# Performance work log

Measured on AMD Instinct MI355X. Metric: run time of the kernel, lower is better.

Reference implementation:

```python
import jax, jax.numpy as jnp
import numpy as np
from jax import lax

B, C, H, W = 2, 64, 192, 192
KS = 3
N = KS * KS
L = 3  # num_gdns (ResBlocks)


def conv2d(x, w, b=None, padding=0):
    out = lax.conv_general_dilated(x, w, (1, 1), [(padding, padding)] * 2,
                                   dimension_numbers=('NCHW', 'OIHW', 'NCHW'))
    if b is not None:
        out = out + b[None, :, None, None]
    return out


def gdn(x, beta, gamma):
    # y = x / sqrt(beta + sum_j gamma_ij x_j^2)  (inverse=False)
    norm = conv2d(x * x, gamma[:, :, None, None], beta)
    return x / jnp.sqrt(norm)


def resblock(x, w1, w2, beta, gamma):
    res = x
    h = jax.nn.celu(gdn(conv2d(x, w1, padding=0), beta, gamma))  # conv1: no pad (H-2)
    return conv2d(h, w2, padding=2) + res  # conv2: pad 2 restores H


def deform_conv(x, offset, w_dc):
    # DCNv1 (pure-pytorch impl): offset (b,2N,h,w), rows first then cols.
    b, c, Hh, Ww = x.shape
    h, w = offset.shape[2], offset.shape[3]
    pad = 1
    xp = jnp.pad(x, ((0, 0), (0, 0), (pad, pad), (pad, pad)))
    Hp, Wp = Hh + 2 * pad, Ww + 2 * pad
    r = (KS - 1) // 2
    knr, knc = jnp.meshgrid(jnp.arange(-r, r + 1), jnp.arange(-r, r + 1), indexing='ij')
    p_n = jnp.concatenate([knr.reshape(-1), knc.reshape(-1)]).astype(x.dtype)  # (2N,)
    gr, gc = jnp.meshgrid(jnp.arange(1, h + 1), jnp.arange(1, w + 1), indexing='ij')
    p0 = jnp.concatenate([jnp.broadcast_to(gr[None], (N, h, w)),
                          jnp.broadcast_to(gc[None], (N, h, w))], 0).astype(x.dtype)  # (2N,h,w)
    p = p0[None] + p_n[None, :, None, None] + offset  # (b,2N,h,w)
    p = jnp.transpose(p, (0, 2, 3, 1))  # (b,h,w,2N)
    pr = jnp.clip(p[..., :N], 0, Hp - 1)
    pc = jnp.clip(p[..., N:], 0, Wp - 1)
    q0 = lax.stop_gradient(jnp.floor(p))
    qr0 = jnp.clip(q0[..., :N], 0, Hp - 1).astype(jnp.int32)
    qc0 = jnp.clip(q0[..., N:], 0, Wp - 1).astype(jnp.int32)
    qr1 = jnp.clip(q0[..., :N] + 1, 0, Hp - 1).astype(jnp.int32)
    qc1 = jnp.clip(q0[..., N:] + 1, 0, Wp - 1).astype(jnp.int32)
    # bilinear weights (match torch impl exactly)
    g_lt = (1 + (qr0 - pr)) * (1 + (qc0 - pc))
    g_rb = (1 - (qr1 - pr)) * (1 - (qc1 - pc))
    g_lb = (1 + (qr0 - pr)) * (1 - (qc1 - pc))
    g_rt = (1 - (qr1 - pr)) * (1 + (qc0 - pc))
    xf = xp.reshape(b, c, Hp * Wp)

    def gather(qr, qc):
        idx = (qr * Wp + qc).reshape(b, -1)  # (b, h*w*N)
        g = jax.vmap(lambda xb, ib: xb[:, ib])(xf, idx)  # (b,c,h*w*N)
        return g.reshape(b, c, h, w, N)

    xo = (g_lt[:, None] * gather(qr0, qc0) + g_rb[:, None] * gather(qr1, qc1)
          + g_lb[:, None] * gather(qr0, qc1) + g_rt[:, None] * gather(qr1, qc0))
    # stride-ks conv over reshaped x_offset == contraction over (c, n)
    wf = w_dc.reshape(w_dc.shape[0], c, N)
    return jnp.einsum('bchwn,ocn->bohw', xo, wf)


def setup_inputs() -> dict:
    key = jax.random.key(0)
    ks = jax.random.split(key, 11)
    f_r = jax.random.normal(ks[0], (B, C, H, W), jnp.float32)
    m_t = jax.random.normal(ks[1], (B, C, H, W), jnp.float32)
    w_pconv = jax.random.normal(ks[2], (2 * N, C, KS, KS), jnp.float32) * 0.01
    b_pconv = jax.random.normal(ks[3], (2 * N,), jnp.float32) * 0.01
    w_dc = jax.random.normal(ks[4], (C, C, KS, KS), jnp.float32) * 0.05
    w_cat = jax.random.normal(ks[5], (C, 2 * C, KS, KS), jnp.float32) * 0.05
    b_cat = jax.random.normal(ks[6], (C,), jnp.float32) * 0.05
    rb_w1 = jax.random.normal(ks[7], (L, C, C, KS, KS), jnp.float32) * 0.01
    rb_w2 = jax.random.normal(ks[8], (L, C, C, KS, KS), jnp.float32) * 0.01
    rb_beta = jax.random.uniform(ks[9], (L, C), jnp.float32) * 0.5 + 0.5
    rb_gamma = jnp.broadcast_to(0.1 * jnp.eye(C, dtype=jnp.float32), (L, C, C)) \
        + jax.random.uniform(ks[10], (L, C, C), jnp.float32) * 0.01
    return {"f_r": f_r, "m_t": m_t, "w_pconv": w_pconv, "b_pconv": b_pconv,
            "w_dc": w_dc, "w_cat": w_cat, "b_cat": b_cat,
            "rb_w1": rb_w1, "rb_w2": rb_w2, "rb_beta": rb_beta, "rb_gamma": rb_gamma}


def reference(f_r, m_t, w_pconv, b_pconv, w_dc, w_cat, b_cat, rb_w1, rb_w2, rb_beta, rb_gamma):
    offset = conv2d(m_t, w_pconv, b_pconv, padding=1)  # (B, 2N, H, W)
    x = deform_conv(f_r, offset, w_dc)                  # (B, C, H, W)
    y = conv2d(jnp.concatenate([x, f_r], axis=1), w_cat, b_cat, padding=1)
    for i in range(L):
        y = resblock(y, rb_w1[i], rb_w2[i], rb_beta[i], rb_gamma[i])
    return y + x
```

## Files before the change

kernel.cpp:

```cpp
#include <hip/hip_runtime.h>

typedef __attribute__((ext_vector_type(8))) __bf16 bf16x8;
typedef __attribute__((ext_vector_type(4))) __bf16 bf16x4;
typedef __attribute__((ext_vector_type(16))) float f32x16;
typedef __attribute__((ext_vector_type(4))) float f32x4;
typedef __attribute__((ext_vector_type(4))) int i32x4;

#define HH 192
#define WW 192
#define HW 36864
#define HW1 36100

#define TCS 144
#define RP66 (66 * TCS)
#define GDNPITCH 144
#define TREG 8704
#define TROW 5120
#define NPREP 1417

__device__ inline f32x16 mfma32(bf16x8 a, bf16x8 b, f32x16 c) {
  return __builtin_amdgcn_mfma_f32_32x32x16_bf16(a, b, c, 0, 0, 0);
}

__device__ inline f32x16 zero16() {
  f32x16 z;
#pragma unroll
  for (int e = 0; e < 16; ++e) z[e] = 0.f;
  return z;
}

__global__ __launch_bounds__(256) void prep_and_nhwc(
    const float* __restrict__ wp, const float* __restrict__ bp,
    const float* __restrict__ wdc, const float* __restrict__ wcat,
    const float* __restrict__ w1, const float* __restrict__ w2,
    const float* __restrict__ gamma,
    __bf16* __restrict__ wpA, __bf16* __restrict__ wdcA,
    __bf16* __restrict__ wcatA, __bf16* __restrict__ w1A,
    __bf16* __restrict__ w2A, __bf16* __restrict__ gA,
    float* __restrict__ bpad,
    const float* __restrict__ fr, const float* __restrict__ mt,
    __bf16* __restrict__ frn, __bf16* __restrict__ mtn) {
  __shared__ __align__(16) __bf16 tile[64 * 72];
  if (blockIdx.x >= NPREP) {
    int rem2 = blockIdx.x - NPREP;
    int tensor = rem2 / 1152, rem = rem2 % 1152;
    int b = rem / 576, p0 = (rem % 576) * 64;
    const float* src = (tensor ? mt : fr) + (size_t)b * 64 * HW;
    __bf16* dst = (tensor ? mtn : frn) + (size_t)b * HW * 64;
    int tid = threadIdx.x, c = tid >> 2, q0 = (tid & 3) * 16;
    const float* sp = src + (size_t)c * HW + p0 + q0;
#pragma unroll
    for (int qq = 0; qq < 4; ++qq) {
      f32x4 v = *(const f32x4*)(sp + qq * 4);
#pragma unroll
      for (int e = 0; e < 4; ++e) tile[(q0 + qq * 4 + e) * 72 + c] = (__bf16)v[e];
    }
    __syncthreads();
    int px = tid >> 2, c0 = (tid & 3) * 16;
    bf16x8 a = *(const bf16x8*)(&tile[px * 72 + c0]);
    bf16x8 b8 = *(const bf16x8*)(&tile[px * 72 + c0 + 8]);
    __bf16* dp = dst + (size_t)(p0 + px) * 64 + c0;
    *(bf16x8*)dp = a;
    *(bf16x8*)(dp + 8) = b8;
    return;
  }
  int i = blockIdx.x * 256 + threadIdx.x;
  if (i < 18432) {
    int j = i & 7, lane = (i >> 3) & 63, kc = (i >> 9) & 3, n = i >> 11;
    int o = lane & 31, c = kc * 16 + ((lane >> 5) << 3) + j;
    wpA[i] = (o < 18) ? (__bf16)wp[(o * 64 + c) * 9 + n] : (__bf16)0.f;
    return;
  }
  i -= 18432;
  if (i < 36864) {
    int j = i & 7, lane = (i >> 3) & 63, ot = (i >> 9) & 1, kc = (i >> 10) & 3, n = i >> 12;
    int o = ot * 32 + (lane & 31), c = kc * 16 + ((lane >> 5) << 3) + j;
    wdcA[i] = (__bf16)wdc[(o * 64 + c) * 9 + n];
    return;
  }
  i -= 36864;
  if (i < 73728) {
    int d = i, j = d & 7; d >>= 3; int lane = d & 63; d >>= 6; int ot = d & 1; d >>= 1;
    int kc = d & 7; int n = d >> 3;
    int o = ot * 32 + (lane & 31), c = kc * 16 + ((lane >> 5) << 3) + j;
    wcatA[i] = (__bf16)wcat[(o * 128 + c) * 9 + n];
    return;
  }
  i -= 73728;
  if (i < 110592) {
    int l = i / 36864, di = i % 36864, d = di;
    int j = d & 7; d >>= 3; int lane = d & 63; d >>= 6; int ot = d & 1; d >>= 1;
    int kc = d & 3; int n = d >> 2;
    int o = ot * 32 + (lane & 31), c = kc * 16 + ((lane >> 5) << 3) + j;
    w1A[l * 36864 + di] = (__bf16)w1[l * 36864 + (o * 64 + c) * 9 + n];
    return;
  }
  i -= 110592;
  if (i < 110592) {
    int l = i / 36864, di = i % 36864, d = di;
    int j = d & 7; d >>= 3; int lane = d & 63; d >>= 6; int ot = d & 1; d >>= 1;
    int kc = d & 3; int n = d >> 2;
    int o = ot * 32 + (lane & 31), c = kc * 16 + ((lane >> 5) << 3) + j;
    w2A[l * 36864 + di] = (__bf16)w2[l * 36864 + (o * 64 + c) * 9 + n];
    return;
  }
  i -= 110592;
  if (i < 12288) {
    int l = i / 4096, di = i % 4096, d = di;
    int j = d & 7; d >>= 3; int lane = d & 63; d >>= 6; int ot = d & 1; d >>= 1;
    int kc = d & 3;
    int o = ot * 32 + (lane & 31), c = kc * 16 + ((lane >> 5) << 3) + j;
    gA[l * 4096 + di] = (__bf16)gamma[l * 4096 + o * 64 + c];
    return;
  }
  i -= 12288;
  if (i < 96) bpad[i] = (i < 18) ? bp[i] : 0.f;
}

template <int ROWS, int COLS, int TPB>
__device__ inline void stage_bf16T(const __bf16* __restrict__ src,
                                   int srcH, int srcW, int row0, int col0,
                                   unsigned char* lds) {
  for (int i = threadIdx.x; i < ROWS * COLS * 8; i += TPB) {
    int r = i / (COLS * 8), rem = i - r * (COLS * 8), j = rem >> 3, u = rem & 7;
    int gr = row0 + r, gc = col0 + j;
    bf16x8 v;
#pragma unroll
    for (int e = 0; e < 8; ++e) v[e] = (__bf16)0.f;
    if (gr >= 0 && gr < srcH && gc >= 0 && gc < srcW)
      v = *(const bf16x8*)(src + ((size_t)gr * srcW + gc) * 64 + u * 8);
    *(bf16x8*)(lds + r * (COLS * TCS) + j * TCS + u * 16) = v;
  }
}

__device__ inline void stage_glds(const __bf16* __restrict__ src, int H, int W,
                                  int gr, int gc0, const __bf16* __restrict__ zpad,
                                  unsigned char* ldsrow, int chunk) {
  int l = threadIdx.x & 63;
  int colg = l >> 3, gsrc = (l & 7) ^ colg;
  int gc = gc0 + chunk * 8 + colg;
  const __bf16* gp = zpad;
  if (gr >= 0 && gr < H && gc >= 0 && gc < W)
    gp = src + ((size_t)gr * W + gc) * 64 + gsrc * 8;
  __builtin_amdgcn_global_load_lds(
      (const __attribute__((address_space(1))) void*)gp,
      (__attribute__((address_space(3))) void*)(ldsrow + chunk * 1024), 16, 0, 0);
}

template <int KCW>
__device__ inline void tapG(const __bf16* __restrict__ aB, int ot,
                            const unsigned char* __restrict__ tile,
                            int n, int koff, f32x16 acc[2]) {
  int lane = threadIdx.x & 63;
  int m = lane & 31, half = lane >> 5;
  int kh = n / 3, kw = n % 3;
  int p = kw + m, p7 = p & 7;
  bf16x8 A[4], B0[4], B1[4];
#pragma unroll
  for (int kc = 0; kc < 4; ++kc)
    A[kc] = *(const bf16x8*)(aB + (size_t)((n * KCW + koff + kc) * 2 + ot) * 512);
#pragma unroll
  for (int kc = 0; kc < 4; ++kc) {
    int gsl = ((kc * 2 + half) ^ p7) << 4;
    B0[kc] = *(const bf16x8*)(tile + (kh + 0) * TROW + p * 128 + gsl);
    B1[kc] = *(const bf16x8*)(tile + (kh + 1) * TROW + p * 128 + gsl);
  }
#pragma unroll
  for (int kc = 0; kc < 4; ++kc) {
    acc[0] = mfma32(A[kc], B0[kc], acc[0]);
    acc[1] = mfma32(A[kc], B1[kc], acc[1]);
  }
}

__device__ inline void merge_write(const f32x16 acc[2], unsigned char* mb) {
  int l = threadIdx.x & 63;
  unsigned char* p = mb + l * 128;
#pragma unroll
  for (int pt = 0; pt < 2; ++pt)
#pragma unroll
    for (int i = 0; i < 4; ++i) {
      f32x4 v;
      v[0] = acc[pt][i * 4 + 0]; v[1] = acc[pt][i * 4 + 1];
      v[2] = acc[pt][i * 4 + 2]; v[3] = acc[pt][i * 4 + 3];
      *(f32x4*)(p + (((pt * 4 + i) ^ (l & 7)) * 16)) = v;
    }
}
__device__ inline void merge_add(f32x16 acc[2], const unsigned char* mb) {
  int l = threadIdx.x & 63;
  const unsigned char* p = mb + l * 128;
#pragma unroll
  for (int pt = 0; pt < 2; ++pt)
#pragma unroll
    for (int i = 0; i < 4; ++i) {
      f32x4 v = *(const f32x4*)(p + (((pt * 4 + i) ^ (l & 7)) * 16));
      acc[pt][i * 4 + 0] += v[0]; acc[pt][i * 4 + 1] += v[1];
      acc[pt][i * 4 + 2] += v[2]; acc[pt][i * 4 + 3] += v[3];
    }
}

__device__ inline void treg_write(const f32x16& a, int ot, unsigned char* reg) {
  int lane = threadIdx.x & 63;
  int m = lane & 31, half = lane >> 5;
#pragma unroll
  for (int g = 0; g < 4; ++g) {
    int o = ot * 32 + half * 4 + g * 8;
    f32x4 v;
    v[0] = a[g * 4 + 0]; v[1] = a[g * 4 + 1];
    v[2] = a[g * 4 + 2]; v[3] = a[g * 4 + 3];
    *(f32x4*)(reg + (m * 68 + o) * 4) = v;
  }
}

__device__ inline void acc32_to_lds(const f32x16 acc[2], unsigned char* reg) {
  int lane = threadIdx.x & 63;
  int colb = lane & 31, half = lane >> 5;
#pragma unroll
  for (int ot = 0; ot < 2; ++ot)
#pragma unroll
    for (int g = 0; g < 4; ++g) {
      int o = ot * 32 + half * 4 + g * 8;
      f32x4 v;
      v[0] = acc[ot][g * 4 + 0]; v[1] = acc[ot][g * 4 + 1];
      v[2] = acc[ot][g * 4 + 2]; v[3] = acc[ot][g * 4 + 3];
      *(f32x4*)(reg + (colb * 68 + o) * 4) = v;
    }
}

__global__ __launch_bounds__(256, 1) void pconv_mfma(
    const __bf16* __restrict__ mtn, const __bf16* __restrict__ wpA,
    const float* __restrict__ bpad, float* __restrict__ off20) {
  __shared__ __align__(16) unsigned char smem[6 * RP66];
  int b = blockIdx.x / 144, r = blockIdx.x % 144, rt = r / 3, ct = r % 3;
  int h0 = rt * 4, w0 = ct * 64;
  int wid = threadIdx.x >> 6, lane = threadIdx.x & 63;
  int colb = lane & 31, half = lane >> 5, kh8 = half << 3;
  stage_bf16T<6, 66, 256>(mtn + (size_t)b * HW * 64, 192, 192, h0 - 1, w0 - 1, smem);
  const __bf16* aB = wpA + lane * 8;
  bf16x8 pcur[4], pnxt[4];
#pragma unroll
  for (int kc = 0; kc < 4; ++kc) pcur[kc] = *(const bf16x8*)(aB + kc * 512);
  __syncthreads();
  f32x16 acc[2];
  acc[0] = zero16(); acc[1] = zero16();
  {
    const unsigned char* bB = smem + wid * RP66 + colb * TCS + kh8 * 2;
#pragma unroll
    for (int n = 0; n < 9; ++n) {
      if (n < 8) {
#pragma unroll
        for (int kc = 0; kc < 4; ++kc)
          pnxt[kc] = *(const bf16x8*)(aB + ((n + 1) * 4 + kc) * 512);
      }
      const int kh = n / 3, kw = n % 3;
#pragma unroll
      for (int kc = 0; kc < 4; ++kc) {
        const unsigned char* bp = bB + kh * RP66 + kw * TCS + kc * 32;
        bf16x8 b0 = *(const bf16x8*)(bp);
        bf16x8 b1 = *(const bf16x8*)(bp + 32 * TCS);
        acc[0] = mfma32(pcur[kc], b0, acc[0]);
        acc[1] = mfma32(pcur[kc], b1, acc[1]);
      }
#pragma unroll
      for (int kc = 0; kc < 4; ++kc) pcur[kc] = pnxt[kc];
    }
  }
  __syncthreads();
  unsigned char* reg = smem + wid * 9216;
#pragma unroll
  for (int pt = 0; pt < 2; ++pt)
#pragma unroll
    for (int g = 0; g < 4; ++g) {
      int o = half * 4 + g * 8;
      f32x4 v;
      v[0] = acc[pt][g * 4 + 0]; v[1] = acc[pt][g * 4 + 1];
      v[2] = acc[pt][g * 4 + 2]; v[3] = acc[pt][g * 4 + 3];
      *(f32x4*)(reg + ((pt * 32 + colb) * 36 + o) * 4) = v;
    }
  __builtin_amdgcn_s_waitcnt(0);
  size_t pix = (size_t)b * HW + (size_t)(h0 + wid) * 192 + w0 + lane;
#pragma unroll
  for (int q = 0; q < 5; ++q) {
    f32x4 v = *(const f32x4*)(reg + (lane * 36 + q * 4) * 4);
    v += *(const f32x4*)(bpad + q * 4);
    *(f32x4*)(off20 + pix * 20 + q * 4) = v;
  }
}

#define GOPITCH 32
#define DTBL (9 * 32 * GOPITCH)
#define DBUF 4608
#define DLDS (DTBL + 4 * DBUF)
__global__ __launch_bounds__(256, 2) void deform_mfma(
    const __bf16* __restrict__ frn, const float* __restrict__ off20,
    const __bf16* __restrict__ wdcA, float* __restrict__ xlow,
    __bf16* __restrict__ xlowb) {
  __shared__ __align__(16) unsigned char smem[DLDS];
  int bid = (blockIdx.x & 7) * 288 + (blockIdx.x >> 3);
  int b = bid / 1152, r = bid % 1152;
  int h = r / 6, s = r % 6;
  int w0 = s * 32;
  int tid = threadIdx.x;
  int wid = tid >> 6, lane = tid & 63;
  int m = lane & 31, half = lane >> 5;
  int pxg = lane >> 3, slot = lane & 7;
  const __bf16* xb = frn + (size_t)b * HW * 64;
  {
    int px = tid & 31, g = tid >> 5;
    int w = w0 + px;
    size_t pixl = (size_t)b * HW + (size_t)h * 192 + w;
    const float* ofp = off20 + pixl * 20;
    for (int n = g; n < 9; n += 8) {
      float offr = ofp[n], offc = ofp[9 + n];
      float pr = (float)(h + 1 + n / 3 - 1) + offr;
      float pc = (float)(w + 1 + n % 3 - 1) + offc;
      float prc = fminf(fmaxf(pr, 0.f), 193.f);
      float pcc = fminf(fmaxf(pc, 0.f), 193.f);
      float f0r = floorf(pr), f0c = floorf(pc);
      int qr0 = (int)fminf(fmaxf(f0r, 0.f), 193.f);
      int qc0 = (int)fminf(fmaxf(f0c, 0.f), 193.f);
      int qr1 = (int)fminf(fmaxf(f0r + 1.f, 0.f), 193.f);
      int qc1 = (int)fminf(fmaxf(f0c + 1.f, 0.f), 193.f);
      float dr0 = 1.f + ((float)qr0 - prc);
      float dr1 = 1.f - ((float)qr1 - prc);
      float dc0 = 1.f + ((float)qc0 - pcc);
      float dc1 = 1.f - ((float)qc1 - pcc);
      int o0, o1, o2, o3; float g0, g1, g2, g3;
      { bool v = (qr0 >= 1 && qr0 <= 192 && qc0 >= 1 && qc0 <= 192);
        o0 = min(max(qr0-1,0),191)*WW + min(max(qc0-1,0),191); g0 = v ? dr0*dc0 : 0.f; }
      { bool v = (qr1 >= 1 && qr1 <= 192 && qc1 >= 1 && qc1 <= 192);
        o1 = min(max(qr1-1,0),191)*WW + min(max(qc1-1,0),191); g1 = v ? dr1*dc1 : 0.f; }
      { bool v = (qr0 >= 1 && qr0 <= 192 && qc1 >= 1 && qc1 <= 192);
        o2 = min(max(qr0-1,0),191)*WW + min(max(qc1-1,0),191); g2 = v ? dr0*dc1 : 0.f; }
      { bool v = (qr1 >= 1 && qr1 <= 192 && qc0 >= 1 && qc0 <= 192);
        o3 = min(max(qr1-1,0),191)*WW + min(max(qc0-1,0),191); g3 = v ? dr1*dc0 : 0.f; }
      unsigned char* dst = smem + (n * 32 + px) * GOPITCH;
      f32x4 gv; gv[0] = g0; gv[1] = g1; gv[2] = g2; gv[3] = g3;
      i32x4 ov; ov[0] = o0; ov[1] = o1; ov[2] = o2; ov[3] = o3;
      *(f32x4*)dst = gv;
      *(i32x4*)(dst + 16) = ov;
    }
  }
  __syncthreads();
  f32x16 acc[2];
  acc[0] = zero16(); acc[1] = zero16();
  const __bf16* aB = wdcA + lane * 8;
  unsigned char* buf = smem + DTBL + wid * DBUF;
  const unsigned char* bB = buf + m * TCS + (half << 3) * 2;
  int n0 = (wid == 0) ? 0 : (wid * 2 + 1);
  int nn = (wid == 0) ? 3 : 2;

  bf16x8 C[4][4];
  f32x4 G[4];
  bf16x8 a[8];

  auto load_tap = [&](int n) {
#pragma unroll
    for (int i = 0; i < 4; ++i) {
      const unsigned char* gp = smem + (size_t)(n * 32 + i * 8 + pxg) * GOPITCH;
      i32x4 oi = *(const i32x4*)(gp + 16);
      G[i] = *(const f32x4*)gp;
#pragma unroll
      for (int j = 0; j < 4; ++j)
        C[i][j] = *(const bf16x8*)(xb + (size_t)oi[j] * 64 + slot * 8);
    }
  };
  auto load_a = [&](int n) {
#pragma unroll
    for (int kc = 0; kc < 4; ++kc) {
      a[kc * 2 + 0] = *(const bf16x8*)(aB + ((n * 4 + kc) * 2 + 0) * 512);
      a[kc * 2 + 1] = *(const bf16x8*)(aB + ((n * 4 + kc) * 2 + 1) * 512);
    }
  };
  auto blend_write = [&]() {
#pragma unroll
    for (int i = 0; i < 4; ++i) {
      bf16x8 ov;
#pragma unroll
      for (int e = 0; e < 8; ++e) {
        float f = G[i][0] * (float)C[i][0][e] + G[i][1] * (float)C[i][1][e] +
                  G[i][2] * (float)C[i][2][e] + G[i][3] * (float)C[i][3][e];
        ov[e] = (__bf16)f;
      }
      *(bf16x8*)(buf + (i * 8 + pxg) * TCS + slot * 16) = ov;
    }
  };
  auto consume = [&]() {
#pragma unroll
    for (int kc = 0; kc < 4; ++kc) {
      bf16x8 b0 = *(const bf16x8*)(bB + kc * 32);
      acc[0] = mfma32(a[kc * 2 + 0], b0, acc[0]);
      acc[1] = mfma32(a[kc * 2 + 1], b0, acc[1]);
    }
  };

  load_tap(n0);
  blend_write();
  for (int t = 1; t < nn; ++t) {
    load_a(n0 + t - 1);
    load_tap(n0 + t);
    consume();
    asm volatile("s_waitcnt lgkmcnt(0)" ::: "memory");
    blend_write();
  }
  load_a(n0 + nn - 1);
  consume();
  __syncthreads();
  if (wid) merge_write(acc, smem + (wid - 1) * 8192);
  __syncthreads();
  if (wid == 0) {
    merge_add(acc, smem);
    merge_add(acc, smem + 8192);
    merge_add(acc, smem + 16384);
    __builtin_amdgcn_s_waitcnt(0);
    unsigned char* reg = smem;
    acc32_to_lds(acc, reg);
    __builtin_amdgcn_s_waitcnt(0);
    int colb = m, ch = half * 32;
    size_t pix = (size_t)b * HW + (size_t)h * 192 + w0 + colb;
    float* dp = xlow + pix * 64 + ch;
    __bf16* dpb = xlowb + pix * 64 + ch;
#pragma unroll
    for (int q = 0; q < 8; ++q) {
      f32x4 v = *(const f32x4*)(reg + (colb * 68 + ch + q * 4) * 4);
      *(f32x4*)(dp + q * 4) = v;
      bf16x4 o8;
#pragma unroll
      for (int e = 0; e < 4; ++e) o8[e] = (__bf16)v[e];
      *(bf16x4*)(dpb + q * 4) = o8;
    }
  }
}

__global__ __launch_bounds__(256, 2) void convcat_mfma(
    const __bf16* __restrict__ xlowb, const __bf16* __restrict__ frn,
    const __bf16* __restrict__ wA, const float* __restrict__ bias,
    const __bf16* __restrict__ zpad, __bf16* __restrict__ y) {
  __shared__ __align__(16) unsigned char smem[2 * 4 * TROW];
  int bid = (blockIdx.x & 7) * 144 + (blockIdx.x >> 3);
  int b = bid / 576, r = bid % 576, rt = r / 6, ct = r % 6;
  int h0 = rt * 2, w0 = ct * 32;
  int tid = threadIdx.x, wid = tid >> 6, lane = tid & 63;
  int ot = wid & 1, g = wid >> 1;
  int m = lane & 31, half = lane >> 5;
  const __bf16* src0 = xlowb + (size_t)b * HW * 64;
  const __bf16* src1 = frn + (size_t)b * HW * 64;
  for (int o = wid; o < 40; o += 4) {
    int t = o / 20, rr = (o % 20) / 5, ck = o % 5;
    stage_glds(t ? src1 : src0, 192, 192, h0 - 1 + rr, w0 - 1, zpad,
               smem + t * (4 * TROW) + rr * TROW, ck);
  }
  __syncthreads();
  const __bf16* aB = wA + lane * 8;
  const unsigned char* tile = smem + g * (4 * TROW);
  int koff = g ? 4 : 0;
  f32x16 acc[2];
  acc[0] = zero16(); acc[1] = zero16();
#pragma unroll
  for (int n = 0; n < 9; ++n) tapG<8>(aB, ot, tile, n, koff, acc);
  __syncthreads();
  if (g == 1) merge_write(acc, smem + ot * 8192);
  __syncthreads();
  if (g == 0) merge_add(acc, smem + ot * 8192);
  __syncthreads();
  if (g == 0) {
    treg_write(acc[0], ot, smem);
    treg_write(acc[1], ot, smem + TREG);
  }
  __syncthreads();
  if (g == 0) {
    const unsigned char* reg = smem + ot * TREG;
    int ch = half * 32;
    int row = h0 + ot;
    __bf16* dp = y + ((size_t)b * HW + (size_t)row * 192 + w0 + m) * 64 + ch;
#pragma unroll
    for (int q = 0; q < 8; ++q) {
      f32x4 v = *(const f32x4*)(reg + (m * 68 + ch + q * 4) * 4);
      v += *(const f32x4*)(bias + ch + q * 4);
      bf16x4 o8;
#pragma unroll
      for (int e = 0; e < 4; ++e) o8[e] = (__bf16)v[e];
      *(bf16x4*)(dp + q * 4) = o8;
    }
  }
}

__global__ __launch_bounds__(256, 2) void conv1gdn_mfma(
    const __bf16* __restrict__ y, const __bf16* __restrict__ w1A,
    const __bf16* __restrict__ gA, const float* __restrict__ beta,
    const __bf16* __restrict__ zpad, __bf16* __restrict__ hbuf) {
  __shared__ __align__(16) unsigned char smem[9216 + 2 * TREG];
  int bid = (blockIdx.x & 7) * 144 + (blockIdx.x >> 3);
  int b = bid / 576, r = bid % 576, rt = r / 6, ct = r % 6;
  int h0 = rt * 2, w0 = ct * 32;
  int tid = threadIdx.x, wid = tid >> 6, lane = tid & 63;
  int ot = wid & 1, g = wid >> 1;
  int m = lane & 31, half = lane >> 5, kh8 = half << 3;
  const __bf16* src = y + (size_t)b * HW * 64;
  for (int o = wid; o < 20; o += 4) {
    int rr = o / 5, ck = o % 5;
    stage_glds(src, 192, 192, h0 + rr, w0, zpad, smem + rr * TROW, ck);
  }
  __syncthreads();
  const __bf16* aB = w1A + lane * 8;
  f32x16 acc[2];
  acc[0] = zero16(); acc[1] = zero16();
  int n0 = g ? 5 : 0, nn = g ? 4 : 5;
  for (int t = 0; t < nn; ++t) tapG<4>(aB, ot, smem, n0 + t, 0, acc);
  __syncthreads();
  if (g == 1) merge_write(acc, smem + ot * 8192);
  __syncthreads();
  if (g == 0) merge_add(acc, smem + ot * 8192);
  __syncthreads();
  unsigned char* gdnreg = smem;
  if (g == 0) {
#pragma unroll
    for (int pt = 0; pt < 2; ++pt)
#pragma unroll
      for (int gg = 0; gg < 4; ++gg) {
        int o = ot * 32 + half * 4 + gg * 8;
        int p = pt * 32 + m;
        bf16x4 s;
#pragma unroll
        for (int e = 0; e < 4; ++e) {
          float x = acc[pt][gg * 4 + e];
          s[e] = (__bf16)(x * x);
        }
        *(bf16x4*)(gdnreg + p * GDNPITCH + o * 2) = s;
      }
  }
  __syncthreads();
  if (g == 0) {
    f32x16 nacc[2];
    nacc[0] = zero16(); nacc[1] = zero16();
    const __bf16* gaB = gA + lane * 8;
    const unsigned char* gb = gdnreg + m * GDNPITCH + kh8 * 2;
#pragma unroll
    for (int kc = 0; kc < 4; ++kc) {
      bf16x8 ga = *(const bf16x8*)(gaB + (kc * 2 + ot) * 512);
      bf16x8 b0 = *(const bf16x8*)(gb + kc * 32);
      bf16x8 b1 = *(const bf16x8*)(gb + 32 * GDNPITCH + kc * 32);
      nacc[0] = mfma32(ga, b0, nacc[0]);
      nacc[1] = mfma32(ga, b1, nacc[1]);
    }
#pragma unroll
    for (int gg = 0; gg < 4; ++gg) {
      f32x4 bet = *(const f32x4*)(beta + ot * 32 + half * 4 + gg * 8);
#pragma unroll
      for (int pt = 0; pt < 2; ++pt)
#pragma unroll
        for (int e = 0; e < 4; ++e) {
          float nv = bet[e] + nacc[pt][gg * 4 + e];
          float hv = acc[pt][gg * 4 + e] * rsqrtf(nv);
          hv = hv > 0.f ? hv : expf(hv) - 1.f;
          acc[pt][gg * 4 + e] = hv;
        }
    }
  }
  __syncthreads();
  if (g == 0) {
    treg_write(acc[0], ot, smem);
    treg_write(acc[1], ot, smem + TREG);
  }
  __syncthreads();
  if (g == 0) {
    const unsigned char* reg = smem + ot * TREG;
    int ch = half * 32;
    int hr = h0 + ot, wcol = w0 + m;
    if (hr < 190 && wcol < 190) {
      __bf16* dp = hbuf + ((size_t)b * HW1 + (size_t)hr * 190 + wcol) * 64 + ch;
#pragma unroll
      for (int q = 0; q < 8; ++q) {
        f32x4 v = *(const f32x4*)(reg + (m * 68 + ch + q * 4) * 4);
        bf16x4 o8;
#pragma unroll
        for (int e = 0; e < 4; ++e) o8[e] = (__bf16)v[e];
        *(bf16x4*)(dp + q * 4) = o8;
      }
    }
  }
}

template <bool LAST>
__global__ __launch_bounds__(256, 2) void conv2_mfma(
    const __bf16* __restrict__ hbuf, const __bf16* __restrict__ w2A,
    const float* __restrict__ xlow, const __bf16* __restrict__ zpad,
    __bf16* __restrict__ y, float* __restrict__ out) {
  __shared__ __align__(16) unsigned char smem[4 * TROW];
  int bid = (blockIdx.x & 7) * 144 + (blockIdx.x >> 3);
  int b = bid / 576, r = bid % 576, rt = r / 6, ct = r % 6;
  int h0 = rt * 2, w0 = ct * 32;
  int tid = threadIdx.x, wid = tid >> 6, lane = tid & 63;
  int ot = wid & 1, g = wid >> 1;
  int m = lane & 31, half = lane >> 5;
  const __bf16* src = hbuf + (size_t)b * HW1 * 64;
  for (int o = wid; o < 20; o += 4) {
    int rr = o / 5, ck = o % 5;
    stage_glds(src, 190, 190, h0 - 2 + rr, w0 - 2, zpad, smem + rr * TROW, ck);
  }
  __syncthreads();
  const __bf16* aB = w2A + lane * 8;
  f32x16 acc[2];
  acc[0] = zero16(); acc[1] = zero16();
  int n0 = g ? 5 : 0, nn = g ? 4 : 5;
  for (int t = 0; t < nn; ++t) tapG<4>(aB, ot, smem, n0 + t, 0, acc);
  __syncthreads();
  if (g == 1) merge_write(acc, smem + ot * 8192);
  __syncthreads();
  if (g == 0) merge_add(acc, smem + ot * 8192);
  __syncthreads();
  if (g == 0) {
    treg_write(acc[0], ot, smem);
    treg_write(acc[1], ot, smem + TREG);
  }
  __syncthreads();
  if (g == 0) {
    unsigned char* reg = smem + ot * TREG;
    int ch = half * 32;
    int row = h0 + ot;
    size_t pix = (size_t)b * HW + (size_t)row * 192 + w0 + m;
    __bf16* yp = y + pix * 64 + ch;
    f32x4 v[8];
#pragma unroll
    for (int q = 0; q < 8; ++q) {
      v[q] = *(const f32x4*)(reg + (m * 68 + ch + q * 4) * 4);
      bf16x4 yv = *(const bf16x4*)(yp + q * 4);
#pragma unroll
      for (int e = 0; e < 4; ++e) v[q][e] += (float)yv[e];
    }
    if (!LAST) {
#pragma unroll
      for (int q = 0; q < 8; ++q) {
        bf16x4 o8;
#pragma unroll
        for (int e = 0; e < 4; ++e) o8[e] = (__bf16)v[q][e];
        *(bf16x4*)(yp + q * 4) = o8;
      }
    } else {
      const float* xp = xlow + pix * 64 + ch;
#pragma unroll
      for (int q = 0; q < 8; ++q) v[q] += *(const f32x4*)(xp + q * 4);
#pragma unroll
      for (int q = 0; q < 8; ++q)
        *(f32x4*)(reg + (m * 68 + ch + q * 4) * 4) = v[q];
      __builtin_amdgcn_s_waitcnt(0);
      int o = lane;
      float* op = out + ((size_t)b * 64 + o) * HW + (size_t)row * 192 + w0;
#pragma unroll
      for (int q = 0; q < 8; ++q) {
        f32x4 s;
#pragma unroll
        for (int e = 0; e < 4; ++e)
          s[e] = *(const float*)(reg + ((q * 4 + e) * 68 + o) * 4);
        *(f32x4*)(op + q * 4) = s;
      }
    }
  }
}

extern "C" void kernel_launch(void* const* d_in, const int* in_sizes, int n_in,
                              void* d_out, int out_size, void* d_ws, size_t ws_size,
                              hipStream_t stream) {
  const float* f_r      = (const float*)d_in[0];
  const float* m_t      = (const float*)d_in[1];
  const float* w_pconv  = (const float*)d_in[2];
  const float* b_pconv  = (const float*)d_in[3];
  const float* w_dc     = (const float*)d_in[4];
  const float* w_cat    = (const float*)d_in[5];
  const float* b_cat    = (const float*)d_in[6];
  const float* rb_w1    = (const float*)d_in[7];
  const float* rb_w2    = (const float*)d_in[8];
  const float* rb_beta  = (const float*)d_in[9];
  const float* rb_gamma = (const float*)d_in[10];
  float* out = (float*)d_out;

  float* ws = (float*)d_ws;
  float*  xlow  = ws;
  __bf16* ybuf  = (__bf16*)(xlow + 4718592);
  __bf16* xlowb = (__bf16*)(xlow + 4718592 + 2359296);
  float*  off20 = xlow + 4718592 + 4718592;
  __bf16* frn   = (__bf16*)(off20 + 1474560);
  __bf16* mtn   = (__bf16*)(off20 + 1474560 + 2359296);
  __bf16* hbuf  = mtn;
  float*  wbase = off20 + 1474560 + 2359296 + 2359296;
  __bf16* wpA   = (__bf16*)wbase;
  __bf16* wdcA  = (__bf16*)(wbase + 9216);
  __bf16* wcatA = (__bf16*)(wbase + 27648);
  __bf16* w1A   = (__bf16*)(wbase + 64512);
  __bf16* w2A   = (__bf16*)(wbase + 119808);
  __bf16* gA    = (__bf16*)(wbase + 175104);
  float*  bpad  = wbase + 181248;
  const __bf16* zpad = (const __bf16*)(bpad + 32);

  prep_and_nhwc<<<NPREP + 2304, 256, 0, stream>>>(
      w_pconv, b_pconv, w_dc, w_cat, rb_w1, rb_w2, rb_gamma,
      wpA, wdcA, wcatA, w1A, w2A, gA, bpad, f_r, m_t, frn, mtn);
  pconv_mfma<<<288, 256, 0, stream>>>(mtn, wpA, bpad, off20);
  deform_mfma<<<2304, 256, 0, stream>>>(frn, off20, wdcA, xlow, xlowb);
  convcat_mfma<<<1152, 256, 0, stream>>>(xlowb, frn, wcatA, b_cat, zpad, ybuf);
  for (int l = 0; l < 3; ++l) {
    conv1gdn_mfma<<<1152, 256, 0, stream>>>(ybuf, w1A + l * 36864, gA + l * 4096,
                                            rb_beta + l * 64, zpad, hbuf);
    if (l < 2)
      conv2_mfma<false><<<1152, 256, 0, stream>>>(hbuf, w2A + l * 36864, xlow, zpad, ybuf, out);
    else
      conv2_mfma<true><<<1152, 256, 0, stream>>>(hbuf, w2A + l * 36864, xlow, zpad, ybuf, out);
  }
}
```

Measured before the change: 275.4 us.

## Split conv waves by output tile and pixel row, drop split-K merge

The convcat, conv1+GDN and conv2 kernels change how work is split across their four waves. Before, two wave groups each covered half of the taps or input channels, and the partial sums were merged through LDS with extra barriers. Now each wave owns one (output-channel tile, pixel row) pair and accumulates the full reduction into a single accumulator, so the merge steps go away and the epilogue is shared by all waves. Lower register use allows launch bounds of 4 blocks per CU, trading some duplicated A-fragment loads for more occupancy and fewer synchronisations.

```diff
diff --git a/kernel.cpp b/kernel.cpp
--- a/kernel.cpp
+++ b/kernel.cpp
@@ -148,54 +148,24 @@
 }
 
 template <int KCW>
-__device__ inline void tapG(const __bf16* __restrict__ aB, int ot,
-                            const unsigned char* __restrict__ tile,
-                            int n, int koff, f32x16 acc[2]) {
+__device__ inline void tapG1(const __bf16* __restrict__ aB, int ot, int pt,
+                             const unsigned char* __restrict__ tile,
+                             int n, int koff, f32x16& acc) {
   int lane = threadIdx.x & 63;
   int m = lane & 31, half = lane >> 5;
   int kh = n / 3, kw = n % 3;
   int p = kw + m, p7 = p & 7;
-  bf16x8 A[4], B0[4], B1[4];
+  bf16x8 A[4], B[4];
 #pragma unroll
   for (int kc = 0; kc < 4; ++kc)
     A[kc] = *(const bf16x8*)(aB + (size_t)((n * KCW + koff + kc) * 2 + ot) * 512);
 #pragma unroll
   for (int kc = 0; kc < 4; ++kc) {
     int gsl = ((kc * 2 + half) ^ p7) << 4;
-    B0[kc] = *(const bf16x8*)(tile + (kh + 0) * TROW + p * 128 + gsl);
-    B1[kc] = *(const bf16x8*)(tile + (kh + 1) * TROW + p * 128 + gsl);
-  }
-#pragma unroll
-  for (int kc = 0; kc < 4; ++kc) {
-    acc[0] = mfma32(A[kc], B0[kc], acc[0]);
-    acc[1] = mfma32(A[kc], B1[kc], acc[1]);
-  }
-}
-
-__device__ inline void merge_write(const f32x16 acc[2], unsigned char* mb) {
-  int l = threadIdx.x & 63;
-  unsigned char* p = mb + l * 128;
-#pragma unroll
-  for (int pt = 0; pt < 2; ++pt)
-#pragma unroll
-    for (int i = 0; i < 4; ++i) {
-      f32x4 v;
-      v[0] = acc[pt][i * 4 + 0]; v[1] = acc[pt][i * 4 + 1];
-      v[2] = acc[pt][i * 4 + 2]; v[3] = acc[pt][i * 4 + 3];
-      *(f32x4*)(p + (((pt * 4 + i) ^ (l & 7)) * 16)) = v;
-    }
-}
-__device__ inline void merge_add(f32x16 acc[2], const unsigned char* mb) {
-  int l = threadIdx.x & 63;
-  const unsigned char* p = mb + l * 128;
-#pragma unroll
-  for (int pt = 0; pt < 2; ++pt)
-#pragma unroll
-    for (int i = 0; i < 4; ++i) {
-      f32x4 v = *(const f32x4*)(p + (((pt * 4 + i) ^ (l & 7)) * 16));
-      acc[pt][i * 4 + 0] += v[0]; acc[pt][i * 4 + 1] += v[1];
-      acc[pt][i * 4 + 2] += v[2]; acc[pt][i * 4 + 3] += v[3];
-    }
+    B[kc] = *(const bf16x8*)(tile + (kh + pt) * TROW + p * 128 + gsl);
+  }
+#pragma unroll
+  for (int kc = 0; kc < 4; ++kc) acc = mfma32(A[kc], B[kc], acc);
 }
 
 __device__ inline void treg_write(const f32x16& a, int ot, unsigned char* reg) {
@@ -209,6 +179,32 @@
     v[2] = a[g * 4 + 2]; v[3] = a[g * 4 + 3];
     *(f32x4*)(reg + (m * 68 + o) * 4) = v;
   }
+}
+
+__device__ inline void merge_write(const f32x16 acc[2], unsigned char* mb) {
+  int l = threadIdx.x & 63;
+  unsigned char* p = mb + l * 128;
+#pragma unroll
+  for (int pt = 0; pt < 2; ++pt)
+#pragma unroll
+    for (int i = 0; i < 4; ++i) {
+      f32x4 v;
+      v[0] = acc[pt][i * 4 + 0]; v[1] = acc[pt][i * 4 + 1];
+      v[2] = acc[pt][i * 4 + 2]; v[3] = acc[pt][i * 4 + 3];
+      *(f32x4*)(p + (((pt * 4 + i) ^ (l & 7)) * 16)) = v;
+    }
+}
+__device__ inline void merge_add(f32x16 acc[2], const unsigned char* mb) {
+  int l = threadIdx.x & 63;
+  const unsigned char* p = mb + l * 128;
+#pragma unroll
+  for (int pt = 0; pt < 2; ++pt)
+#pragma unroll
+    for (int i = 0; i < 4; ++i) {
+      f32x4 v = *(const f32x4*)(p + (((pt * 4 + i) ^ (l & 7)) * 16));
+      acc[pt][i * 4 + 0] += v[0]; acc[pt][i * 4 + 1] += v[1];
+      acc[pt][i * 4 + 2] += v[2]; acc[pt][i * 4 + 3] += v[3];
+    }
 }
 
 __device__ inline void acc32_to_lds(const f32x16 acc[2], unsigned char* reg) {
@@ -431,7 +427,7 @@
   }
 }
 
-__global__ __launch_bounds__(256, 2) void convcat_mfma(
+__global__ __launch_bounds__(256, 4) void convcat_mfma(
     const __bf16* __restrict__ xlowb, const __bf16* __restrict__ frn,
     const __bf16* __restrict__ wA, const float* __restrict__ bias,
     const __bf16* __restrict__ zpad, __bf16* __restrict__ y) {
@@ -440,7 +436,7 @@
   int b = bid / 576, r = bid % 576, rt = r / 6, ct = r % 6;
   int h0 = rt * 2, w0 = ct * 32;
   int tid = threadIdx.x, wid = tid >> 6, lane = tid & 63;
-  int ot = wid & 1, g = wid >> 1;
+  int pt = wid & 1, ot = wid >> 1;
   int m = lane & 31, half = lane >> 5;
   const __bf16* src0 = xlowb + (size_t)b * HW * 64;
   const __bf16* src1 = frn + (size_t)b * HW * 64;
@@ -451,29 +447,21 @@
   }
   __syncthreads();
   const __bf16* aB = wA + lane * 8;
-  const unsigned char* tile = smem + g * (4 * TROW);
-  int koff = g ? 4 : 0;
-  f32x16 acc[2];
-  acc[0] = zero16(); acc[1] = zero16();
-#pragma unroll
-  for (int n = 0; n < 9; ++n) tapG<8>(aB, ot, tile, n, koff, acc);
-  __syncthreads();
-  if (g == 1) merge_write(acc, smem + ot * 8192);
-  __syncthreads();
-  if (g == 0) merge_add(acc, smem + ot * 8192);
-  __syncthreads();
-  if (g == 0) {
-    treg_write(acc[0], ot, smem);
-    treg_write(acc[1], ot, smem + TREG);
-  }
-  __syncthreads();
-  if (g == 0) {
-    const unsigned char* reg = smem + ot * TREG;
-    int ch = half * 32;
-    int row = h0 + ot;
+  f32x16 acc = zero16();
+#pragma unroll
+  for (int n = 0; n < 9; ++n) tapG1<8>(aB, ot, pt, smem, n, 0, acc);
+#pragma unroll
+  for (int n = 0; n < 9; ++n) tapG1<8>(aB, ot, pt, smem + 4 * TROW, n, 4, acc);
+  __syncthreads();
+  treg_write(acc, ot, smem + pt * TREG);
+  __syncthreads();
+  {
+    const unsigned char* reg = smem + pt * TREG;
+    int ch = ot * 32 + half * 16;
+    int row = h0 + pt;
     __bf16* dp = y + ((size_t)b * HW + (size_t)row * 192 + w0 + m) * 64 + ch;
 #pragma unroll
-    for (int q = 0; q < 8; ++q) {
+    for (int q = 0; q < 4; ++q) {
       f32x4 v = *(const f32x4*)(reg + (m * 68 + ch + q * 4) * 4);
       v += *(const f32x4*)(bias + ch + q * 4);
       bf16x4 o8;
@@ -484,7 +472,7 @@
   }
 }
 
-__global__ __launch_bounds__(256, 2) void conv1gdn_mfma(
+__global__ __launch_bounds__(256, 4) void conv1gdn_mfma(
     const __bf16* __restrict__ y, const __bf16* __restrict__ w1A,
     const __bf16* __restrict__ gA, const float* __restrict__ beta,
     const __bf16* __restrict__ zpad, __bf16* __restrict__ hbuf) {
@@ -493,7 +481,7 @@
   int b = bid / 576, r = bid % 576, rt = r / 6, ct = r % 6;
   int h0 = rt * 2, w0 = ct * 32;
   int tid = threadIdx.x, wid = tid >> 6, lane = tid & 63;
-  int ot = wid & 1, g = wid >> 1;
+  int pt = wid & 1, ot = wid >> 1;
   int m = lane & 31, half = lane >> 5, kh8 = half << 3;
   const __bf16* src = y + (size_t)b * HW * 64;
   for (int o = wid; o < 20; o += 4) {
@@ -502,74 +490,58 @@
   }
   __syncthreads();
   const __bf16* aB = w1A + lane * 8;
-  f32x16 acc[2];
-  acc[0] = zero16(); acc[1] = zero16();
-  int n0 = g ? 5 : 0, nn = g ? 4 : 5;
-  for (int t = 0; t < nn; ++t) tapG<4>(aB, ot, smem, n0 + t, 0, acc);
-  __syncthreads();
-  if (g == 1) merge_write(acc, smem + ot * 8192);
-  __syncthreads();
-  if (g == 0) merge_add(acc, smem + ot * 8192);
+  f32x16 acc = zero16();
+#pragma unroll
+  for (int n = 0; n < 9; ++n) tapG1<4>(aB, ot, pt, smem, n, 0, acc);
   __syncthreads();
   unsigned char* gdnreg = smem;
-  if (g == 0) {
-#pragma unroll
-    for (int pt = 0; pt < 2; ++pt)
-#pragma unroll
-      for (int gg = 0; gg < 4; ++gg) {
-        int o = ot * 32 + half * 4 + gg * 8;
-        int p = pt * 32 + m;
-        bf16x4 s;
-#pragma unroll
-        for (int e = 0; e < 4; ++e) {
-          float x = acc[pt][gg * 4 + e];
-          s[e] = (__bf16)(x * x);
-        }
-        *(bf16x4*)(gdnreg + p * GDNPITCH + o * 2) = s;
-      }
-  }
-  __syncthreads();
-  if (g == 0) {
-    f32x16 nacc[2];
-    nacc[0] = zero16(); nacc[1] = zero16();
+  {
+    int p = pt * 32 + m;
+#pragma unroll
+    for (int gg = 0; gg < 4; ++gg) {
+      int o = ot * 32 + half * 4 + gg * 8;
+      bf16x4 s;
+#pragma unroll
+      for (int e = 0; e < 4; ++e) {
+        float x = acc[gg * 4 + e];
+        s[e] = (__bf16)(x * x);
+      }
+      *(bf16x4*)(gdnreg + p * GDNPITCH + o * 2) = s;
+    }
+  }
+  __syncthreads();
+  {
+    f32x16 nacc = zero16();
     const __bf16* gaB = gA + lane * 8;
-    const unsigned char* gb = gdnreg + m * GDNPITCH + kh8 * 2;
+    const unsigned char* gb = gdnreg + (pt * 32 + m) * GDNPITCH + kh8 * 2;
 #pragma unroll
     for (int kc = 0; kc < 4; ++kc) {
       bf16x8 ga = *(const bf16x8*)(gaB + (kc * 2 + ot) * 512);
       bf16x8 b0 = *(const bf16x8*)(gb + kc * 32);
-      bf16x8 b1 = *(const bf16x8*)(gb + 32 * GDNPITCH + kc * 32);
-      nacc[0] = mfma32(ga, b0, nacc[0]);
-      nacc[1] = mfma32(ga, b1, nacc[1]);
+      nacc = mfma32(ga, b0, nacc);
     }
 #pragma unroll
     for (int gg = 0; gg < 4; ++gg) {
       f32x4 bet = *(const f32x4*)(beta + ot * 32 + half * 4 + gg * 8);
 #pragma unroll
-      for (int pt = 0; pt < 2; ++pt)
-#pragma unroll
-        for (int e = 0; e < 4; ++e) {
-          float nv = bet[e] + nacc[pt][gg * 4 + e];
-          float hv = acc[pt][gg * 4 + e] * rsqrtf(nv);
-          hv = hv > 0.f ? hv : expf(hv) - 1.f;
-          acc[pt][gg * 4 + e] = hv;
-        }
-    }
-  }
-  __syncthreads();
-  if (g == 0) {
-    treg_write(acc[0], ot, smem);
-    treg_write(acc[1], ot, smem + TREG);
-  }
-  __syncthreads();
-  if (g == 0) {
-    const unsigned char* reg = smem + ot * TREG;
-    int ch = half * 32;
-    int hr = h0 + ot, wcol = w0 + m;
+      for (int e = 0; e < 4; ++e) {
+        float nv = bet[e] + nacc[gg * 4 + e];
+        float hv = acc[gg * 4 + e] * rsqrtf(nv);
+        hv = hv > 0.f ? hv : expf(hv) - 1.f;
+        acc[gg * 4 + e] = hv;
+      }
+    }
+  }
+  treg_write(acc, ot, smem + 9216 + pt * TREG);
+  __syncthreads();
+  {
+    const unsigned char* reg = smem + 9216 + pt * TREG;
+    int ch = ot * 32 + half * 16;
+    int hr = h0 + pt, wcol = w0 + m;
     if (hr < 190 && wcol < 190) {
       __bf16* dp = hbuf + ((size_t)b * HW1 + (size_t)hr * 190 + wcol) * 64 + ch;
 #pragma unroll
-      for (int q = 0; q < 8; ++q) {
+      for (int q = 0; q < 4; ++q) {
         f32x4 v = *(const f32x4*)(reg + (m * 68 + ch + q * 4) * 4);
         bf16x4 o8;
 #pragma unroll
@@ -581,7 +553,7 @@
 }
 
 template <bool LAST>
-__global__ __launch_bounds__(256, 2) void conv2_mfma(
+__global__ __launch_bounds__(256, 4) void conv2_mfma(
     const __bf16* __restrict__ hbuf, const __bf16* __restrict__ w2A,
     const float* __restrict__ xlow, const __bf16* __restrict__ zpad,
     __bf16* __restrict__ y, float* __restrict__ out) {
@@ -590,7 +562,7 @@
   int b = bid / 576, r = bid % 576, rt = r / 6, ct = r % 6;
   int h0 = rt * 2, w0 = ct * 32;
   int tid = threadIdx.x, wid = tid >> 6, lane = tid & 63;
-  int ot = wid & 1, g = wid >> 1;
+  int pt = wid & 1, ot = wid >> 1;
   int m = lane & 31, half = lane >> 5;
   const __bf16* src = hbuf + (size_t)b * HW1 * 64;
   for (int o = wid; o < 20; o += 4) {
@@ -599,29 +571,21 @@
   }
   __syncthreads();
   const __bf16* aB = w2A + lane * 8;
-  f32x16 acc[2];
-  acc[0] = zero16(); acc[1] = zero16();
-  int n0 = g ? 5 : 0, nn = g ? 4 : 5;
-  for (int t = 0; t < nn; ++t) tapG<4>(aB, ot, smem, n0 + t, 0, acc);
-  __syncthreads();
-  if (g == 1) merge_write(acc, smem + ot * 8192);
-  __syncthreads();
-  if (g == 0) merge_add(acc, smem + ot * 8192);
-  __syncthreads();
-  if (g == 0) {
-    treg_write(acc[0], ot, smem);
-    treg_write(acc[1], ot, smem + TREG);
-  }
-  __syncthreads();
-  if (g == 0) {
-    unsigned char* reg = smem + ot * TREG;
-    int ch = half * 32;
-    int row = h0 + ot;
+  f32x16 acc = zero16();
+#pragma unroll
+  for (int n = 0; n < 9; ++n) tapG1<4>(aB, ot, pt, smem, n, 0, acc);
+  __syncthreads();
+  treg_write(acc, ot, smem + pt * TREG);
+  __syncthreads();
+  {
+    unsigned char* reg = smem + pt * TREG;
+    int ch = ot * 32 + half * 16;
+    int row = h0 + pt;
     size_t pix = (size_t)b * HW + (size_t)row * 192 + w0 + m;
     __bf16* yp = y + pix * 64 + ch;
-    f32x4 v[8];
-#pragma unroll
-    for (int q = 0; q < 8; ++q) {
+    f32x4 v[4];
+#pragma unroll
+    for (int q = 0; q < 4; ++q) {
       v[q] = *(const f32x4*)(reg + (m * 68 + ch + q * 4) * 4);
       bf16x4 yv = *(const bf16x4*)(yp + q * 4);
 #pragma unroll
@@ -629,7 +593,7 @@
     }
     if (!LAST) {
 #pragma unroll
-      for (int q = 0; q < 8; ++q) {
+      for (int q = 0; q < 4; ++q) {
         bf16x4 o8;
 #pragma unroll
         for (int e = 0; e < 4; ++e) o8[e] = (__bf16)v[q][e];
@@ -638,15 +602,16 @@
     } else {
       const float* xp = xlow + pix * 64 + ch;
 #pragma unroll
-      for (int q = 0; q < 8; ++q) v[q] += *(const f32x4*)(xp + q * 4);
-#pragma unroll
-      for (int q = 0; q < 8; ++q)
+      for (int q = 0; q < 4; ++q) v[q] += *(const f32x4*)(xp + q * 4);
+#pragma unroll
+      for (int q = 0; q < 4; ++q)
         *(f32x4*)(reg + (m * 68 + ch + q * 4) * 4) = v[q];
-      __builtin_amdgcn_s_waitcnt(0);
+      __syncthreads();
       int o = lane;
       float* op = out + ((size_t)b * 64 + o) * HW + (size_t)row * 192 + w0;
 #pragma unroll
-      for (int q = 0; q < 8; ++q) {
+      for (int qq = 0; qq < 4; ++qq) {
+        int q = ot * 4 + qq;
         f32x4 s;
 #pragma unroll
         for (int e = 0; e < 4; ++e)
```

Result: faster. 258.0 us (-6.3%).
